# Kernel tuning notes

Hardware: AMD Instinct MI355X
Metric: run time of the kernel (lower is better)

Reference implementation:

```python
import jax, jax.numpy as jnp
import numpy as np

N, D, C = 4096, 512, 64
MARGIN = 1.0
INF = jnp.float32(1e30)


def setup_inputs() -> dict:
    key = jax.random.key(0)
    k1, k2 = jax.random.split(key)
    embeddings = jax.random.normal(k1, (N, D), dtype=jnp.float32)
    targets = jax.random.randint(k2, (N,), 0, C)
    return {"embeddings": embeddings, "targets": targets}


def _triplet_loss(embeddings, targets, margin=MARGIN):
    # Squared pairwise distances [N, N] (differentiable, used for the loss)
    sq_norms = jnp.sum(embeddings * embeddings, axis=1)
    sq_dist = jnp.maximum(
        sq_norms[:, None] + sq_norms[None, :] - 2.0 * (embeddings @ embeddings.T), 0.0
    )
    # Euclidean distances for mining only (index selection is non-differentiable in torch)
    dist = jnp.sqrt(jax.lax.stop_gradient(sq_dist))

    same = targets[:, None] == targets[None, :]  # [N, N] same-label mask

    # Hardest negative per anchor: argmax_k (d_ap - d_ak + margin) == argmin_k d_ak over negatives
    neg_dist = jnp.where(same, INF, dist)
    n_idx = jnp.argmin(neg_dist, axis=1)   # [N] hardest negative index per anchor
    min_neg = jnp.min(neg_dist, axis=1)    # [N] its euclidean distance

    idx = jnp.arange(dist.shape[0])
    # anchor-positive pairs: same label, a < p (torch.combinations on sorted indices)
    pair_mask = same & (idx[:, None] < idx[None, :])
    # triplet kept only if mined loss (euclidean) strictly positive
    valid = pair_mask & (dist - min_neg[:, None] + margin > 0)

    ap_sq = sq_dist                         # [N, N] squared anchor-positive distances
    an_sq = sq_dist[idx, n_idx]             # [N]   squared anchor-hard-negative distances
    losses = jax.nn.relu(ap_sq - an_sq[:, None] + margin)

    cnt = jnp.sum(valid)
    denom = jnp.maximum(cnt, 1).astype(losses.dtype)
    loss = jnp.sum(jnp.where(valid, losses, 0.0)) / denom

    correct = jnp.sum(valid & (ap_sq < an_sq[:, None]))
    accuracy = correct.astype(jnp.float32) / jnp.maximum(cnt, 1).astype(jnp.float32)
    return loss, accuracy


def reference(embeddings, targets):
    return _triplet_loss(embeddings, targets)
```

## Files before the change

kernel.cpp:

```cpp
#include <hip/hip_runtime.h>

#define N 4096
#define D 512
#define C 64
#define MARGIN 1.0f
#define TILE 64
#define BK 64
#define SKB 144
#define NTILES (N / TILE)
#define NTRI (NTILES * (NTILES + 1) / 2)
#define FINF 3.0e38f
#define MAXM 112

#define NSLOT 64
#define SLOTW 16

typedef __attribute__((ext_vector_type(8))) short short8;
typedef __attribute__((ext_vector_type(4))) float floatx4;

__device__ __forceinline__ unsigned short f2bf(float f) {
  unsigned int u = __float_as_uint(f);
  u += 0x7FFFu + ((u >> 16) & 1u);
  return (unsigned short)(u >> 16);
}

__global__ __launch_bounds__(256) void prep_kernel(const float* __restrict__ E,
                                                   const int* __restrict__ targets,
                                                   unsigned short* __restrict__ Ebf,
                                                   float* __restrict__ norms,
                                                   unsigned int* __restrict__ an_sq_bits,
                                                   int* __restrict__ cls_mem,
                                                   int* __restrict__ cls_off) {
  const int row = blockIdx.x;
  const int tid = threadIdx.x;
  if (row == N) {
    __shared__ unsigned int cnt[C];
    __shared__ unsigned int base[C];
    if (tid < C) cnt[tid] = 0;
    __syncthreads();
    for (int i = tid; i < N; i += 256) atomicAdd(&cnt[targets[i]], 1);
    __syncthreads();
    if (tid == 0) {
      unsigned int s = 0;
      for (int c = 0; c < C; c++) { base[c] = s; s += cnt[c]; }
    }
    __syncthreads();
    if (tid < C) cnt[tid] = base[tid];
    __syncthreads();
    for (int i = tid; i < N; i += 256) {
      const int c = targets[i];
      const unsigned int p = atomicAdd(&cnt[c], 1);
      cls_mem[p] = i;
    }
    if (tid < C) cls_off[tid] = (int)base[tid];
    if (tid == 0) cls_off[C] = N;
    return;
  }
  if (row < 16) an_sq_bits[row * 256 + tid] = 0x7F800000u;
  const float2 v = reinterpret_cast<const float2*>(E + (size_t)row * D)[tid];
  float s = v.x * v.x + v.y * v.y;
  unsigned int packed = ((unsigned int)f2bf(v.y) << 16) | (unsigned int)f2bf(v.x);
  reinterpret_cast<unsigned int*>(Ebf + (size_t)row * D)[tid] = packed;
  for (int off = 32; off > 0; off >>= 1) s += __shfl_down(s, off);
  __shared__ float wsum[4];
  if ((tid & 63) == 0) wsum[tid >> 6] = s;
  __syncthreads();
  if (tid == 0) norms[row] = wsum[0] + wsum[1] + wsum[2] + wsum[3];
}

__global__ __launch_bounds__(256, 8) void gemm_min_kernel(const unsigned short* __restrict__ Ebf,
                                                          const float* __restrict__ norms,
                                                          const int* __restrict__ targets,
                                                          unsigned int* __restrict__ an_sq_bits) {
  const int u = blockIdx.x;
  int i = (int)((sqrtf(8.0f * (float)u + 1.0f) - 1.0f) * 0.5f);
  while ((i + 1) * (i + 2) / 2 <= u) ++i;
  while (i * (i + 1) / 2 > u) --i;
  const int tm = u - i * (i + 1) / 2;
  const int tn = i;

  __shared__ alignas(16) unsigned char As[TILE * SKB];
  __shared__ alignas(16) unsigned char Bs[TILE * SKB];
  __shared__ float s_rmin[2][TILE];
  __shared__ float s_cmin[2][TILE];

  const int tid = threadIdx.x;
  const int wave = tid >> 6, lane = tid & 63;
  const int quad = lane >> 4, l16 = lane & 15;
  const int wr = wave >> 1, wc = wave & 1;
  const int rowBase = tm * TILE, colBase = tn * TILE;

  floatx4 acc[2][2];
#pragma unroll
  for (int a = 0; a < 2; a++)
#pragma unroll
    for (int b = 0; b < 2; b++) acc[a][b] = (floatx4){0.f, 0.f, 0.f, 0.f};

  for (int k0 = 0; k0 < D; k0 += BK) {
#pragma unroll
    for (int s = tid; s < TILE * 8; s += 256) {
      const int r = s >> 3, q = s & 7;
      const uint4 va = *reinterpret_cast<const uint4*>(&Ebf[(size_t)(rowBase + r) * D + k0 + q * 8]);
      *reinterpret_cast<uint4*>(&As[r * SKB + q * 16]) = va;
      const uint4 vb = *reinterpret_cast<const uint4*>(&Ebf[(size_t)(colBase + r) * D + k0 + q * 8]);
      *reinterpret_cast<uint4*>(&Bs[r * SKB + q * 16]) = vb;
    }
    __syncthreads();
#pragma unroll
    for (int ks = 0; ks < 2; ks++) {
      short8 af[2], bf[2];
#pragma unroll
      for (int s = 0; s < 2; s++) {
        af[s] = *reinterpret_cast<const short8*>(&As[(wr * 32 + s * 16 + l16) * SKB + ks * 64 + quad * 16]);
        bf[s] = *reinterpret_cast<const short8*>(&Bs[(wc * 32 + s * 16 + l16) * SKB + ks * 64 + quad * 16]);
      }
#pragma unroll
      for (int sm = 0; sm < 2; sm++)
#pragma unroll
        for (int sn = 0; sn < 2; sn++)
          acc[sm][sn] = __builtin_amdgcn_mfma_f32_16x16x32_bf16(af[sm], bf[sn], acc[sm][sn], 0, 0, 0);
    }
    __syncthreads();
  }

  int tcol[2];
  float ncol[2];
#pragma unroll
  for (int sn = 0; sn < 2; sn++) {
    const int gc = colBase + wc * 32 + sn * 16 + l16;
    tcol[sn] = targets[gc];
    ncol[sn] = norms[gc];
  }
  float colmin[2] = {FINF, FINF};
#pragma unroll
  for (int sm = 0; sm < 2; sm++) {
#pragma unroll
    for (int r = 0; r < 4; r++) {
      const int rloc = wr * 32 + sm * 16 + quad * 4 + r;
      const int grow = rowBase + rloc;
      const int trow = targets[grow];
      const float nrow = norms[grow];
      float rowmin = FINF;
#pragma unroll
      for (int sn = 0; sn < 2; sn++) {
        const float sq = fmaxf(nrow + ncol[sn] - 2.0f * acc[sm][sn][r], 0.0f);
        if (tcol[sn] != trow) {
          rowmin = fminf(rowmin, sq);
          colmin[sn] = fminf(colmin[sn], sq);
        }
      }
#pragma unroll
      for (int off = 1; off < 16; off <<= 1) rowmin = fminf(rowmin, __shfl_xor(rowmin, off));
      if (l16 == 0) s_rmin[wc][rloc] = rowmin;
    }
  }
#pragma unroll
  for (int sn = 0; sn < 2; sn++) {
    float cm = colmin[sn];
    cm = fminf(cm, __shfl_xor(cm, 16));
    cm = fminf(cm, __shfl_xor(cm, 32));
    if (quad == 0) s_cmin[wr][wc * 32 + sn * 16 + l16] = cm;
  }
  __syncthreads();
  if (tid < TILE) {
    const float m = fminf(s_rmin[0][tid], s_rmin[1][tid]);
    if (m < FINF) atomicMin(&an_sq_bits[rowBase + tid], __float_as_uint(m));
  } else if (tid < 2 * TILE) {
    const int c = tid - TILE;
    const float m = fminf(s_cmin[0][c], s_cmin[1][c]);
    if (m < FINF) atomicMin(&an_sq_bits[colBase + c], __float_as_uint(m));
  }
}

__global__ __launch_bounds__(256) void loss_kernel(const unsigned short* __restrict__ Ebf,
                                                   const float* __restrict__ norms,
                                                   const unsigned int* __restrict__ an_sq_bits,
                                                   const int* __restrict__ cls_mem,
                                                   const int* __restrict__ cls_off,
                                                   float* __restrict__ accs) {
  const int c = blockIdx.x;
  const int tid = threadIdx.x, wave = tid >> 6, lane = tid & 63;
  const int quad = lane >> 4, l16 = lane & 15;
  const int o = cls_off[c];
  const int s_c = min(cls_off[c + 1] - o, MAXM);

  __shared__ alignas(16) unsigned char S[MAXM * SKB];
  __shared__ int l_mem[MAXM];
  __shared__ float l_norm[MAXM];
  __shared__ float l_an[MAXM];
  __shared__ signed char pti[28], ptj[28];
  __shared__ float s_sum[4];
  __shared__ unsigned int s_cnt[4], s_cor[4];

  if (tid < s_c) {
    const int m = cls_mem[o + tid];
    l_mem[tid] = m;
    l_norm[tid] = norms[m];
    l_an[tid] = __uint_as_float(an_sq_bits[m]);
  }
  const int nt = (s_c + 15) >> 4;
  const int npairs = nt * (nt + 1) / 2;
  if (tid == 0) {
    int w = 0;
    for (int ti = 0; ti < nt; ti++)
      for (int tj = ti; tj < nt; tj++) { pti[w] = (signed char)ti; ptj[w] = (signed char)tj; w++; }
  }
  __syncthreads();

  floatx4 pacc[7];
#pragma unroll
  for (int pp = 0; pp < 7; pp++) pacc[pp] = (floatx4){0.f, 0.f, 0.f, 0.f};

  for (int k0 = 0; k0 < D; k0 += BK) {
    for (int s = tid; s < s_c * 8; s += 256) {
      const int r = s >> 3, q = s & 7;
      *reinterpret_cast<uint4*>(&S[r * SKB + q * 16]) =
          *reinterpret_cast<const uint4*>(&Ebf[(size_t)l_mem[r] * D + k0 + q * 8]);
    }
    __syncthreads();
#pragma unroll
    for (int pp = 0; pp < 7; pp++) {
      const int p = wave + 4 * pp;
      if (p < npairs) {
        const int ti = pti[p], tj = ptj[p];
#pragma unroll
        for (int ks = 0; ks < 2; ks++) {
          const short8 af = *reinterpret_cast<const short8*>(&S[(ti * 16 + l16) * SKB + ks * 64 + quad * 16]);
          const short8 bf = *reinterpret_cast<const short8*>(&S[(tj * 16 + l16) * SKB + ks * 64 + quad * 16]);
          pacc[pp] = __builtin_amdgcn_mfma_f32_16x16x32_bf16(af, bf, pacc[pp], 0, 0, 0);
        }
      }
    }
    __syncthreads();
  }

  float bsum = 0.f;
  unsigned int bcnt = 0, bcor = 0;
#pragma unroll
  for (int pp = 0; pp < 7; pp++) {
    const int p = wave + 4 * pp;
    if (p < npairs) {
      const int ti = pti[p], tj = ptj[p];
#pragma unroll
      for (int r = 0; r < 4; r++) {
        const int i_loc = ti * 16 + quad * 4 + r;
        const int j_loc = tj * 16 + l16;
        if (i_loc < s_c && j_loc < s_c && (ti < tj || i_loc < j_loc)) {
          const int oi = l_mem[i_loc], oj = l_mem[j_loc];
          const float sq = fmaxf(l_norm[i_loc] + l_norm[j_loc] - 2.0f * pacc[pp][r], 0.0f);
          const float an = (oi < oj) ? l_an[i_loc] : l_an[j_loc];
          if (sqrtf(sq) - sqrtf(an) + MARGIN > 0.0f) {
            bcnt++;
            bsum += fmaxf(sq - an + MARGIN, 0.0f);
            if (sq < an) bcor++;
          }
        }
      }
    }
  }
#pragma unroll
  for (int off = 32; off > 0; off >>= 1) {
    bsum += __shfl_down(bsum, off);
    bcnt += __shfl_down(bcnt, off);
    bcor += __shfl_down(bcor, off);
  }
  if (lane == 0) { s_sum[wave] = bsum; s_cnt[wave] = bcnt; s_cor[wave] = bcor; }
  __syncthreads();
  if (tid == 0) {
    float* slot = accs + (size_t)c * SLOTW;
    slot[0] = s_sum[0] + s_sum[1] + s_sum[2] + s_sum[3];
    ((unsigned int*)slot)[1] = s_cnt[0] + s_cnt[1] + s_cnt[2] + s_cnt[3];
    ((unsigned int*)slot)[2] = s_cor[0] + s_cor[1] + s_cor[2] + s_cor[3];
  }
}

__global__ void finalize_kernel(const float* __restrict__ accs, float* __restrict__ out) {
  const int lane = threadIdx.x;
  float sum = accs[(size_t)lane * SLOTW + 0];
  unsigned int cnt = ((const unsigned int*)accs)[(size_t)lane * SLOTW + 1];
  unsigned int cor = ((const unsigned int*)accs)[(size_t)lane * SLOTW + 2];
  for (int off = 32; off > 0; off >>= 1) {
    sum += __shfl_down(sum, off);
    cnt += __shfl_down(cnt, off);
    cor += __shfl_down(cor, off);
  }
  if (lane == 0) {
    const float denom = (float)(cnt > 0u ? cnt : 1u);
    out[0] = sum / denom;
    out[1] = (float)cor / denom;
  }
}

extern "C" void kernel_launch(void* const* d_in, const int* in_sizes, int n_in,
                              void* d_out, int out_size, void* d_ws, size_t ws_size,
                              hipStream_t stream) {
  const float* E = (const float*)d_in[0];
  const int* targets = (const int*)d_in[1];
  float* out = (float*)d_out;
  char* ws = (char*)d_ws;
  size_t off = 0;
  unsigned short* Ebf = (unsigned short*)(ws + off); off += (size_t)N * D * 2;
  float* norms = (float*)(ws + off); off += (size_t)N * 4;
  unsigned int* an_sq = (unsigned int*)(ws + off); off += (size_t)N * 4;
  float* accs = (float*)(ws + off); off += (size_t)NSLOT * SLOTW * 4;
  int* cls_mem = (int*)(ws + off); off += (size_t)N * 4;
  int* cls_off = (int*)(ws + off);

  prep_kernel<<<dim3(N + 1), dim3(256), 0, stream>>>(E, targets, Ebf, norms, an_sq, cls_mem, cls_off);
  gemm_min_kernel<<<dim3(NTRI), dim3(256), 0, stream>>>(Ebf, norms, targets, an_sq);
  loss_kernel<<<dim3(C), dim3(256), 0, stream>>>(Ebf, norms, an_sq, cls_mem, cls_off, accs);
  finalize_kernel<<<1, 64, 0, stream>>>(accs, out);
}
```

Measured before the change: 113.5 us.

## Use direct global-to-LDS loads with XOR swizzle and fuse finalize into loss kernel

The GEMM tile loads now go straight from global memory into LDS through global_load_lds, with XOR-swizzled 128-byte rows in place of padded rows. This removes the register staging and the separate LDS store instructions. The finalize kernel is dropped: the last loss block, found through an atomic counter, does the final reduction, which saves one kernel launch. Launch bounds also change from 8 to 6 waves. The risks are the ordering and atomic-fence logic of the last-block pattern and possible LDS bank conflicts from the swizzle.

Result: faster. 110.9 us (-2.3%).

```diff
diff --git a/kernel.cpp b/kernel.cpp
--- a/kernel.cpp
+++ b/kernel.cpp
@@ -6,13 +6,12 @@
 #define MARGIN 1.0f
 #define TILE 64
 #define BK 64
-#define SKB 144
+#define ROWB 128
 #define NTILES (N / TILE)
 #define NTRI (NTILES * (NTILES + 1) / 2)
 #define FINF 3.0e38f
 #define MAXM 112
-
-#define NSLOT 64
+#define SKB 144
 #define SLOTW 16
 
 typedef __attribute__((ext_vector_type(8))) short short8;
@@ -22,6 +21,12 @@
   unsigned int u = __float_as_uint(f);
   u += 0x7FFFu + ((u >> 16) & 1u);
   return (unsigned short)(u >> 16);
+}
+
+__device__ __forceinline__ void gload_lds16(const void* g, void* l) {
+  __builtin_amdgcn_global_load_lds(
+      (const __attribute__((address_space(1))) unsigned int*)g,
+      (__attribute__((address_space(3))) unsigned int*)l, 16, 0, 0);
 }
 
 __global__ __launch_bounds__(256) void prep_kernel(const float* __restrict__ E,
@@ -30,12 +35,14 @@
                                                    float* __restrict__ norms,
                                                    unsigned int* __restrict__ an_sq_bits,
                                                    int* __restrict__ cls_mem,
-                                                   int* __restrict__ cls_off) {
+                                                   int* __restrict__ cls_off,
+                                                   unsigned int* __restrict__ done) {
   const int row = blockIdx.x;
   const int tid = threadIdx.x;
   if (row == N) {
     __shared__ unsigned int cnt[C];
     __shared__ unsigned int base[C];
+    if (tid == 0) *done = 0u;
     if (tid < C) cnt[tid] = 0;
     __syncthreads();
     for (int i = tid; i < N; i += 256) atomicAdd(&cnt[targets[i]], 1);
@@ -68,7 +75,7 @@
   if (tid == 0) norms[row] = wsum[0] + wsum[1] + wsum[2] + wsum[3];
 }
 
-__global__ __launch_bounds__(256, 8) void gemm_min_kernel(const unsigned short* __restrict__ Ebf,
+__global__ __launch_bounds__(256, 6) void gemm_min_kernel(const unsigned short* __restrict__ Ebf,
                                                           const float* __restrict__ norms,
                                                           const int* __restrict__ targets,
                                                           unsigned int* __restrict__ an_sq_bits) {
@@ -79,8 +86,8 @@
   const int tm = u - i * (i + 1) / 2;
   const int tn = i;
 
-  __shared__ alignas(16) unsigned char As[TILE * SKB];
-  __shared__ alignas(16) unsigned char Bs[TILE * SKB];
+  __shared__ alignas(16) unsigned char As[TILE * ROWB];
+  __shared__ alignas(16) unsigned char Bs[TILE * ROWB];
   __shared__ float s_rmin[2][TILE];
   __shared__ float s_cmin[2][TILE];
 
@@ -90,35 +97,46 @@
   const int wr = wave >> 1, wc = wave & 1;
   const int rowBase = tm * TILE, colBase = tn * TILE;
 
+  const int lr = lane >> 3;
+  const int lq = (lane & 7) ^ lr;
+  const int lofs = lr * (D * 2) + lq * 16;
+  const unsigned char* gA = (const unsigned char*)Ebf + (size_t)rowBase * (D * 2);
+  const unsigned char* gB = (const unsigned char*)Ebf + (size_t)colBase * (D * 2);
+
+  const int swz = l16 & 7;
+  int rA[2], rB[2], cq[2];
+#pragma unroll
+  for (int s = 0; s < 2; s++) {
+    rA[s] = (wr * 32 + s * 16 + l16) * ROWB;
+    rB[s] = (wc * 32 + s * 16 + l16) * ROWB;
+  }
+#pragma unroll
+  for (int ks = 0; ks < 2; ks++) cq[ks] = ((ks * 4 + quad) ^ swz) * 16;
+
   floatx4 acc[2][2];
 #pragma unroll
   for (int a = 0; a < 2; a++)
 #pragma unroll
     for (int b = 0; b < 2; b++) acc[a][b] = (floatx4){0.f, 0.f, 0.f, 0.f};
 
-  for (int k0 = 0; k0 < D; k0 += BK) {
-#pragma unroll
-    for (int s = tid; s < TILE * 8; s += 256) {
-      const int r = s >> 3, q = s & 7;
-      const uint4 va = *reinterpret_cast<const uint4*>(&Ebf[(size_t)(rowBase + r) * D + k0 + q * 8]);
-      *reinterpret_cast<uint4*>(&As[r * SKB + q * 16]) = va;
-      const uint4 vb = *reinterpret_cast<const uint4*>(&Ebf[(size_t)(colBase + r) * D + k0 + q * 8]);
-      *reinterpret_cast<uint4*>(&Bs[r * SKB + q * 16]) = vb;
+  for (int k0b = 0; k0b < D * 2; k0b += BK * 2) {
+#pragma unroll
+    for (int t = 0; t < 2; t++) {
+      const int g = wave + t * 4;
+      gload_lds16(gA + (size_t)g * 8 * (D * 2) + lofs + k0b, As + g * 1024);
+      gload_lds16(gB + (size_t)g * 8 * (D * 2) + lofs + k0b, Bs + g * 1024);
     }
     __syncthreads();
 #pragma unroll
     for (int ks = 0; ks < 2; ks++) {
-      short8 af[2], bf[2];
-#pragma unroll
-      for (int s = 0; s < 2; s++) {
-        af[s] = *reinterpret_cast<const short8*>(&As[(wr * 32 + s * 16 + l16) * SKB + ks * 64 + quad * 16]);
-        bf[s] = *reinterpret_cast<const short8*>(&Bs[(wc * 32 + s * 16 + l16) * SKB + ks * 64 + quad * 16]);
-      }
-#pragma unroll
-      for (int sm = 0; sm < 2; sm++)
-#pragma unroll
-        for (int sn = 0; sn < 2; sn++)
-          acc[sm][sn] = __builtin_amdgcn_mfma_f32_16x16x32_bf16(af[sm], bf[sn], acc[sm][sn], 0, 0, 0);
+      const short8 af0 = *reinterpret_cast<const short8*>(As + rA[0] + cq[ks]);
+      const short8 af1 = *reinterpret_cast<const short8*>(As + rA[1] + cq[ks]);
+      const short8 bf0 = *reinterpret_cast<const short8*>(Bs + rB[0] + cq[ks]);
+      const short8 bf1 = *reinterpret_cast<const short8*>(Bs + rB[1] + cq[ks]);
+      acc[0][0] = __builtin_amdgcn_mfma_f32_16x16x32_bf16(af0, bf0, acc[0][0], 0, 0, 0);
+      acc[0][1] = __builtin_amdgcn_mfma_f32_16x16x32_bf16(af0, bf1, acc[0][1], 0, 0, 0);
+      acc[1][0] = __builtin_amdgcn_mfma_f32_16x16x32_bf16(af1, bf0, acc[1][0], 0, 0, 0);
+      acc[1][1] = __builtin_amdgcn_mfma_f32_16x16x32_bf16(af1, bf1, acc[1][1], 0, 0, 0);
     }
     __syncthreads();
   }
@@ -177,7 +195,9 @@
                                                    const unsigned int* __restrict__ an_sq_bits,
                                                    const int* __restrict__ cls_mem,
                                                    const int* __restrict__ cls_off,
-                                                   float* __restrict__ accs) {
+                                                   float* __restrict__ accs,
+                                                   unsigned int* __restrict__ done,
+                                                   float* __restrict__ out) {
   const int c = blockIdx.x;
   const int tid = threadIdx.x, wave = tid >> 6, lane = tid & 63;
   const int quad = lane >> 4, l16 = lane & 15;
@@ -191,6 +211,7 @@
   __shared__ signed char pti[28], ptj[28];
   __shared__ float s_sum[4];
   __shared__ unsigned int s_cnt[4], s_cor[4];
+  __shared__ int s_last;
 
   if (tid < s_c) {
     const int m = cls_mem[o + tid];
@@ -268,26 +289,31 @@
   __syncthreads();
   if (tid == 0) {
     float* slot = accs + (size_t)c * SLOTW;
-    slot[0] = s_sum[0] + s_sum[1] + s_sum[2] + s_sum[3];
-    ((unsigned int*)slot)[1] = s_cnt[0] + s_cnt[1] + s_cnt[2] + s_cnt[3];
-    ((unsigned int*)slot)[2] = s_cor[0] + s_cor[1] + s_cor[2] + s_cor[3];
-  }
-}
-
-__global__ void finalize_kernel(const float* __restrict__ accs, float* __restrict__ out) {
-  const int lane = threadIdx.x;
-  float sum = accs[(size_t)lane * SLOTW + 0];
-  unsigned int cnt = ((const unsigned int*)accs)[(size_t)lane * SLOTW + 1];
-  unsigned int cor = ((const unsigned int*)accs)[(size_t)lane * SLOTW + 2];
-  for (int off = 32; off > 0; off >>= 1) {
-    sum += __shfl_down(sum, off);
-    cnt += __shfl_down(cnt, off);
-    cor += __shfl_down(cor, off);
-  }
-  if (lane == 0) {
-    const float denom = (float)(cnt > 0u ? cnt : 1u);
-    out[0] = sum / denom;
-    out[1] = (float)cor / denom;
+    atomicExch((unsigned int*)&slot[0], __float_as_uint(s_sum[0] + s_sum[1] + s_sum[2] + s_sum[3]));
+    atomicExch((unsigned int*)&slot[1], s_cnt[0] + s_cnt[1] + s_cnt[2] + s_cnt[3]);
+    atomicExch((unsigned int*)&slot[2], s_cor[0] + s_cor[1] + s_cor[2] + s_cor[3]);
+    __threadfence();
+    s_last = (atomicAdd(done, 1u) == C - 1);
+  }
+  __syncthreads();
+  if (s_last) {
+    __threadfence();
+    if (tid < C) {
+      float sum = __uint_as_float(atomicAdd((unsigned int*)&accs[(size_t)tid * SLOTW + 0], 0u));
+      unsigned int cnt = atomicAdd((unsigned int*)&accs[(size_t)tid * SLOTW + 1], 0u);
+      unsigned int cor = atomicAdd((unsigned int*)&accs[(size_t)tid * SLOTW + 2], 0u);
+#pragma unroll
+      for (int off = 32; off > 0; off >>= 1) {
+        sum += __shfl_down(sum, off);
+        cnt += __shfl_down(cnt, off);
+        cor += __shfl_down(cor, off);
+      }
+      if (tid == 0) {
+        const float denom = (float)(cnt > 0u ? cnt : 1u);
+        out[0] = sum / denom;
+        out[1] = (float)cor / denom;
+      }
+    }
   }
 }
 
@@ -302,12 +328,12 @@
   unsigned short* Ebf = (unsigned short*)(ws + off); off += (size_t)N * D * 2;
   float* norms = (float*)(ws + off); off += (size_t)N * 4;
   unsigned int* an_sq = (unsigned int*)(ws + off); off += (size_t)N * 4;
-  float* accs = (float*)(ws + off); off += (size_t)NSLOT * SLOTW * 4;
+  float* accs = (float*)(ws + off); off += (size_t)C * SLOTW * 4;
   int* cls_mem = (int*)(ws + off); off += (size_t)N * 4;
-  int* cls_off = (int*)(ws + off);
-
-  prep_kernel<<<dim3(N + 1), dim3(256), 0, stream>>>(E, targets, Ebf, norms, an_sq, cls_mem, cls_off);
+  int* cls_off = (int*)(ws + off); off += 512;
+  unsigned int* done = (unsigned int*)(ws + off);
+
+  prep_kernel<<<dim3(N + 1), dim3(256), 0, stream>>>(E, targets, Ebf, norms, an_sq, cls_mem, cls_off, done);
   gemm_min_kernel<<<dim3(NTRI), dim3(256), 0, stream>>>(Ebf, norms, targets, an_sq);
-  loss_kernel<<<dim3(C), dim3(256), 0, stream>>>(Ebf, norms, an_sq, cls_mem, cls_off, accs);
-  finalize_kernel<<<1, 64, 0, stream>>>(accs, out);
-}
+  loss_kernel<<<dim3(C), dim3(256), 0, stream>>>(Ebf, norms, an_sq, cls_mem, cls_off, accs, done, out);
+}
```
